# Kernel optimization log

Hardware: AMD Instinct MI355X
Metric: run time of the kernel (lower is better)

Reference implementation:

```python
import jax, jax.numpy as jnp
import numpy as np

B, D, NUM_IDS = 4096, 256, 100000
MARGIN = 0.5


def setup_inputs() -> dict:
    key = jax.random.key(0)
    k1, k2, k3, k4 = jax.random.split(key, 4)
    ftr = jax.random.normal(k1, (B, D), dtype=jnp.float32)
    teachor_ftr = jax.random.normal(k2, (B, D), dtype=jnp.float32)
    prototypes = jax.random.normal(k3, (NUM_IDS, D), dtype=jnp.float32)
    label = jax.random.randint(k4, (B,), 0, NUM_IDS, dtype=jnp.int64)
    return {"ftr": ftr, "teachor_ftr": teachor_ftr, "prototypes": prototypes, "label": label}


def reference(ftr, teachor_ftr, prototypes, label):
    # y = prototypes[label] : [B, D]
    y = prototypes[label]
    # similarity = ftr @ ftr.T : [B, B]
    sim = jnp.einsum('bd,kd->bk', ftr, ftr)
    n = ftr.shape[0]
    idx = jnp.arange(n)
    # Original: ascending sort, take first batch index i with i != label[row].
    # Equivalent: argmin of sim with positions where batch-index == label masked out.
    masked = jnp.where(idx[None, :] == label[:, None], jnp.inf, sim)
    neg_i = jnp.argmin(masked, axis=1)          # [B]
    neg = ftr[neg_i]                            # [B, D]
    pos_d = jnp.sum((ftr - y) ** 2, axis=1)     # [B]
    neg_d = jnp.sum((ftr - neg) ** 2, axis=1)   # [B]
    losses = jax.nn.relu(pos_d - neg_d + MARGIN)
    # sum(losses) / len(losses)
    return jnp.mean(losses)
```

## Files before the change

kernel.cpp:

```cpp
#include <hip/hip_runtime.h>
#include <hip/hip_bf16.h>
#include <stdint.h>


typedef _Float16 f16;
typedef _Float16 f16x4 __attribute__((ext_vector_type(4)));
typedef _Float16 f16x8 __attribute__((ext_vector_type(8)));
typedef float f32x4 __attribute__((ext_vector_type(4)));
typedef unsigned long long u64;

__device__ __forceinline__ u64 float_key(float x) {
    unsigned int u = __float_as_uint(x);
    u = (u & 0x80000000u) ? ~u : (u | 0x80000000u);
    return (u64)u;
}

__device__ __forceinline__ u64 shfl_xor_u64(u64 v, int mask) {
    unsigned int lo = (unsigned int)(v & 0xFFFFFFFFULL);
    unsigned int hi = (unsigned int)(v >> 32);
    lo = __shfl_xor(lo, mask, 64);
    hi = __shfl_xor(hi, mask, 64);
    return ((u64)hi << 32) | (u64)lo;
}

__device__ __forceinline__ void async_load16(const void* g, void* lds) {
    __builtin_amdgcn_global_load_lds(
        (__attribute__((address_space(1))) void*)(g),
        (__attribute__((address_space(3))) void*)(lds),
        16, 0, 0);
}

__global__ __launch_bounds__(256) void prep_kernel(
    const float* __restrict__ x, f16* __restrict__ F,
    u64* __restrict__ best, float* __restrict__ out, int B, int D)
{
    int gid = blockIdx.x * blockDim.x + threadIdx.x;
    int n4 = (B * D) >> 2;
    if (gid < n4) {
        float4 v = ((const float4*)x)[gid];
        f16x4 h = { (f16)v.x, (f16)v.y, (f16)v.z, (f16)v.w };
        ((f16x4*)F)[gid] = h;
    }
    if (gid < B) best[gid] = ~0ULL;
    if (gid == 0) out[0] = 0.0f;
}

__global__ __launch_bounds__(256, 3) void sim_mfma_kernel(
    const f16* __restrict__ F, const int* __restrict__ label,
    u64* __restrict__ best, int B, int K)
{
    __shared__ __align__(16) f16 sA[128 * 64];
    __shared__ __align__(16) f16 sB[128 * 64];
    __shared__ int sLabR[128];
    __shared__ int sLabC[128];

    int bi = blockIdx.x;
    int by = (int)((sqrtf(8.0f * (float)bi + 1.0f) - 1.0f) * 0.5f);
    while ((by + 1) * (by + 2) / 2 <= bi) ++by;
    while (by * (by + 1) / 2 > bi) --by;
    const int bx = bi - by * (by + 1) / 2;

    const int row0 = by * 128;
    const int col0 = bx * 128;

    const int tid  = threadIdx.x;
    const int lane = tid & 63;
    const int w    = tid >> 6;

    if (tid < 128) sLabR[tid] = label[row0 + tid];
    else           sLabC[tid - 128] = label[col0 + (tid - 128)];

    const int srow   = w * 32 + (lane >> 3);
    const int schunk = ((lane & 7) ^ (lane >> 3)) << 3;
    const f16* gA = F + (size_t)(row0 + srow) * K + schunk;
    const f16* gB = F + (size_t)(col0 + srow) * K + schunk;
    f16* lA0 = sA + (w * 32) * 64;
    f16* lB0 = sB + (w * 32) * 64;

    f32x4 acc[4][4];
#pragma unroll
    for (int i = 0; i < 4; ++i)
#pragma unroll
        for (int j = 0; j < 4; ++j) acc[i][j] = (f32x4){0.f, 0.f, 0.f, 0.f};

    const int wr = (w >> 1) * 64;
    const int wc = (w & 1) * 64;
    const int qk = lane >> 4;
    const int ln = lane & 15;

    for (int k0 = 0; k0 < K; k0 += 64) {
        __syncthreads();
#pragma unroll
        for (int t = 0; t < 4; ++t) {
            async_load16(gA + (size_t)(t * 8) * K + k0, lA0 + t * 8 * 64);
            async_load16(gB + (size_t)(t * 8) * K + k0, lB0 + t * 8 * 64);
        }
        __syncthreads();

#pragma unroll
        for (int kk = 0; kk < 2; ++kk) {
            const int q  = kk * 4 + qk;
            const int cs = ((q ^ (ln & 7)) << 3);
            f16x8 aF[4], bF[4];
#pragma unroll
            for (int f = 0; f < 4; ++f) {
                const int lrA = wr + f * 16 + ln;
                const int lrB = wc + f * 16 + ln;
                aF[f] = __builtin_bit_cast(f16x8, *(const uint4*)&sA[lrA * 64 + cs]);
                bF[f] = __builtin_bit_cast(f16x8, *(const uint4*)&sB[lrB * 64 + cs]);
            }
#pragma unroll
            for (int i = 0; i < 4; ++i)
#pragma unroll
                for (int j = 0; j < 4; ++j)
                    acc[i][j] = __builtin_amdgcn_mfma_f32_16x16x32_f16(
                        aF[i], bF[j], acc[i][j], 0, 0, 0);
        }
    }

#pragma unroll
    for (int i = 0; i < 4; ++i) {
#pragma unroll
        for (int reg = 0; reg < 4; ++reg) {
            const int lr  = wr + i * 16 + qk * 4 + reg;
            const int lab = sLabR[lr];
            u64 bl = ~0ULL;
#pragma unroll
            for (int j = 0; j < 4; ++j) {
                const int c = col0 + wc + j * 16 + ln;
                u64 key = (float_key(acc[i][j][reg]) << 32) | (unsigned int)c;
                if (c != lab && key < bl) bl = key;
            }
#pragma unroll
            for (int off = 1; off < 16; off <<= 1) {
                u64 o = shfl_xor_u64(bl, off);
                if (o < bl) bl = o;
            }
            if (ln == 0) atomicMin(&best[row0 + lr], bl);
        }
    }

#pragma unroll
    for (int j = 0; j < 4; ++j) {
        const int cl  = wc + j * 16 + ln;
        const int lab = sLabC[cl];
        u64 bl = ~0ULL;
#pragma unroll
        for (int i = 0; i < 4; ++i) {
#pragma unroll
            for (int reg = 0; reg < 4; ++reg) {
                const int rg = row0 + wr + i * 16 + qk * 4 + reg;
                u64 key = (float_key(acc[i][j][reg]) << 32) | (unsigned int)rg;
                if (rg != lab && key < bl) bl = key;
            }
        }
#pragma unroll
        for (int off = 16; off < 64; off <<= 1) {
            u64 o = shfl_xor_u64(bl, off);
            if (o < bl) bl = o;
        }
        if (qk == 0) atomicMin(&best[col0 + cl], bl);
    }
}

__global__ __launch_bounds__(256) void loss_kernel(
    const float* __restrict__ ftr, const float* __restrict__ proto,
    const int* __restrict__ label, const u64* __restrict__ best,
    float* __restrict__ out, int B, int D, float inv_b)
{
    const int gid  = blockIdx.x * blockDim.x + threadIdx.x;
    const int row  = gid >> 6;
    const int lane = gid & 63;
    if (row >= B) return;

    const int lab = label[row];
    const int neg = (int)(unsigned int)(best[row] & 0xFFFFFFFFULL);

    float pd = 0.0f, nd = 0.0f;
    for (int d = lane * 4; d < D; d += 256) {
        float4 f = *(const float4*)(ftr   + (size_t)row * D + d);
        float4 y = *(const float4*)(proto + (size_t)lab * D + d);
        float4 n = *(const float4*)(ftr   + (size_t)neg * D + d);
        float dx = f.x - y.x, dy = f.y - y.y, dz = f.z - y.z, dw = f.w - y.w;
        pd += dx * dx + dy * dy + dz * dz + dw * dw;
        dx = f.x - n.x; dy = f.y - n.y; dz = f.z - n.z; dw = f.w - n.w;
        nd += dx * dx + dy * dy + dz * dz + dw * dw;
    }
#pragma unroll
    for (int off = 32; off >= 1; off >>= 1) {
        pd += __shfl_xor(pd, off, 64);
        nd += __shfl_xor(nd, off, 64);
    }
    if (lane == 0) {
        float l = pd - nd + 0.5f;
        if (l > 0.0f) atomicAdd(out, l * inv_b);
    }
}

extern "C" void kernel_launch(void* const* d_in, const int* in_sizes, int n_in,
                              void* d_out, int out_size, void* d_ws, size_t ws_size,
                              hipStream_t stream) {
    const float* ftr   = (const float*)d_in[0];
    const float* proto = (const float*)d_in[2];
    const int*   label = (const int*)d_in[3];

    const int B = in_sizes[3];
    const int D = in_sizes[0] / B;

    u64* best = (u64*)d_ws;
    size_t off = ((size_t)B * 8 + 255) & ~(size_t)255;
    f16* F = (f16*)((char*)d_ws + off);
    float* out = (float*)d_out;

    const int prep_threads = (B * D) >> 2;
    prep_kernel<<<(prep_threads + 255) / 256, 256, 0, stream>>>(ftr, F, best, out, B, D);

    const int nb = B / 128;
    const int ntri = nb * (nb + 1) / 2;
    sim_mfma_kernel<<<ntri, 256, 0, stream>>>(F, label, best, B, D);

    loss_kernel<<<(B * 64 + 255) / 256, 256, 0, stream>>>(ftr, proto, label, best, out, B, D,
                                                          1.0f / (float)B);
}
```

Baseline: 152.9 us.

## Fuse prep, similarity and loss into one cooperative kernel with grid syncs

Merges the three kernels into a single cooperative launch that separates the prep, similarity and loss phases with grid-wide syncs, falling back to separate launches when the triangular grid cannot be co-resident. It also stages per-row and per-column argmin candidates in shared memory so each block issues one atomicMin per row or column instead of one per wave. Diagonal tiles now skip the redundant column pass. Launch overhead and atomic traffic go down, but grid syncs, per-call occupancy queries and grid-stride loops over a smaller grid in the prep and loss phases are added.

```diff
diff --git a/kernel.cpp b/kernel.cpp
--- a/kernel.cpp
+++ b/kernel.cpp
@@ -1,6 +1,9 @@
 #include <hip/hip_runtime.h>
 #include <hip/hip_bf16.h>
+#include <hip/hip_cooperative_groups.h>
 #include <stdint.h>
+
+namespace cg = cooperative_groups;
 
 
 typedef _Float16 f16;
@@ -30,22 +33,24 @@
         16, 0, 0);
 }
 
-__global__ __launch_bounds__(256) void prep_kernel(
+__device__ __forceinline__ void phase_prep(
     const float* __restrict__ x, f16* __restrict__ F,
     u64* __restrict__ best, float* __restrict__ out, int B, int D)
 {
-    int gid = blockIdx.x * blockDim.x + threadIdx.x;
-    int n4 = (B * D) >> 2;
-    if (gid < n4) {
-        float4 v = ((const float4*)x)[gid];
+    const int nthreads = gridDim.x * blockDim.x;
+    const int gid = blockIdx.x * blockDim.x + threadIdx.x;
+    const int n4 = (B * D) >> 2;
+    for (int i = gid; i < n4; i += nthreads) {
+        float4 v = ((const float4*)x)[i];
         f16x4 h = { (f16)v.x, (f16)v.y, (f16)v.z, (f16)v.w };
-        ((f16x4*)F)[gid] = h;
-    }
-    if (gid < B) best[gid] = ~0ULL;
-    if (gid == 0) out[0] = 0.0f;
-}
-
-__global__ __launch_bounds__(256, 3) void sim_mfma_kernel(
+        ((f16x4*)F)[i] = h;
+    }
+    for (int i = gid; i < B; i += nthreads) best[i] = ~0ULL;
+    if (gid == 0)
+        __hip_atomic_store(out, 0.0f, __ATOMIC_RELAXED, __HIP_MEMORY_SCOPE_AGENT);
+}
+
+__device__ __forceinline__ void phase_sim(
     const f16* __restrict__ F, const int* __restrict__ label,
     u64* __restrict__ best, int B, int K)
 {
@@ -53,12 +58,15 @@
     __shared__ __align__(16) f16 sB[128 * 64];
     __shared__ int sLabR[128];
     __shared__ int sLabC[128];
+    __shared__ u64 sRedR[2][128];
+    __shared__ u64 sRedC[2][128];
 
     int bi = blockIdx.x;
     int by = (int)((sqrtf(8.0f * (float)bi + 1.0f) - 1.0f) * 0.5f);
     while ((by + 1) * (by + 2) / 2 <= bi) ++by;
     while (by * (by + 1) / 2 > bi) --by;
     const int bx = bi - by * (by + 1) / 2;
+    const bool diag = (bx == by);
 
     const int row0 = by * 128;
     const int col0 = bx * 128;
@@ -104,10 +112,8 @@
             f16x8 aF[4], bF[4];
 #pragma unroll
             for (int f = 0; f < 4; ++f) {
-                const int lrA = wr + f * 16 + ln;
-                const int lrB = wc + f * 16 + ln;
-                aF[f] = __builtin_bit_cast(f16x8, *(const uint4*)&sA[lrA * 64 + cs]);
-                bF[f] = __builtin_bit_cast(f16x8, *(const uint4*)&sB[lrB * 64 + cs]);
+                aF[f] = __builtin_bit_cast(f16x8, *(const uint4*)&sA[(wr + f * 16 + ln) * 64 + cs]);
+                bF[f] = __builtin_bit_cast(f16x8, *(const uint4*)&sB[(wc + f * 16 + ln) * 64 + cs]);
             }
 #pragma unroll
             for (int i = 0; i < 4; ++i)
@@ -136,65 +142,113 @@
                 u64 o = shfl_xor_u64(bl, off);
                 if (o < bl) bl = o;
             }
-            if (ln == 0) atomicMin(&best[row0 + lr], bl);
-        }
-    }
-
-#pragma unroll
-    for (int j = 0; j < 4; ++j) {
-        const int cl  = wc + j * 16 + ln;
-        const int lab = sLabC[cl];
-        u64 bl = ~0ULL;
-#pragma unroll
-        for (int i = 0; i < 4; ++i) {
-#pragma unroll
-            for (int reg = 0; reg < 4; ++reg) {
-                const int rg = row0 + wr + i * 16 + qk * 4 + reg;
-                u64 key = (float_key(acc[i][j][reg]) << 32) | (unsigned int)rg;
-                if (rg != lab && key < bl) bl = key;
-            }
-        }
-#pragma unroll
-        for (int off = 16; off < 64; off <<= 1) {
-            u64 o = shfl_xor_u64(bl, off);
-            if (o < bl) bl = o;
-        }
-        if (qk == 0) atomicMin(&best[col0 + cl], bl);
-    }
+            if (ln == 0) sRedR[w & 1][lr] = bl;
+        }
+    }
+
+    if (!diag) {
+#pragma unroll
+        for (int j = 0; j < 4; ++j) {
+            const int cl  = wc + j * 16 + ln;
+            const int lab = sLabC[cl];
+            u64 bl = ~0ULL;
+#pragma unroll
+            for (int i = 0; i < 4; ++i) {
+#pragma unroll
+                for (int reg = 0; reg < 4; ++reg) {
+                    const int rg = row0 + wr + i * 16 + qk * 4 + reg;
+                    u64 key = (float_key(acc[i][j][reg]) << 32) | (unsigned int)rg;
+                    if (rg != lab && key < bl) bl = key;
+                }
+            }
+            u64 o = shfl_xor_u64(bl, 16); if (o < bl) bl = o;
+            o     = shfl_xor_u64(bl, 32); if (o < bl) bl = o;
+            if (qk == 0) sRedC[w >> 1][cl] = bl;
+        }
+    }
+
+    __syncthreads();
+    if (tid < 128) {
+        u64 a = sRedR[0][tid], b = sRedR[1][tid];
+        atomicMin(&best[row0 + tid], a < b ? a : b);
+    } else if (!diag) {
+        const int c = tid - 128;
+        u64 a = sRedC[0][c], b = sRedC[1][c];
+        atomicMin(&best[col0 + c], a < b ? a : b);
+    }
+}
+
+__device__ __forceinline__ void phase_loss(
+    const float* __restrict__ ftr, const float* __restrict__ proto,
+    const int* __restrict__ label, u64* __restrict__ best,
+    float* __restrict__ out, int B, int D, float inv_b)
+{
+    const int nwaves = gridDim.x * (blockDim.x >> 6);
+    const int wid0   = blockIdx.x * (blockDim.x >> 6) + (threadIdx.x >> 6);
+    const int lane   = threadIdx.x & 63;
+
+    for (int row = wid0; row < B; row += nwaves) {
+        const int lab = label[row];
+        const u64 bk  = __hip_atomic_load(&best[row], __ATOMIC_RELAXED,
+                                          __HIP_MEMORY_SCOPE_AGENT);
+        const int neg = (int)(unsigned int)(bk & 0xFFFFFFFFULL);
+
+        float pd = 0.0f, nd = 0.0f;
+        for (int d = lane * 4; d < D; d += 256) {
+            float4 f = *(const float4*)(ftr   + (size_t)row * D + d);
+            float4 y = *(const float4*)(proto + (size_t)lab * D + d);
+            float4 n = *(const float4*)(ftr   + (size_t)neg * D + d);
+            float dx = f.x - y.x, dy = f.y - y.y, dz = f.z - y.z, dw = f.w - y.w;
+            pd += dx * dx + dy * dy + dz * dz + dw * dw;
+            dx = f.x - n.x; dy = f.y - n.y; dz = f.z - n.z; dw = f.w - n.w;
+            nd += dx * dx + dy * dy + dz * dz + dw * dw;
+        }
+#pragma unroll
+        for (int off = 32; off >= 1; off >>= 1) {
+            pd += __shfl_xor(pd, off, 64);
+            nd += __shfl_xor(nd, off, 64);
+        }
+        if (lane == 0) {
+            float l = pd - nd + 0.5f;
+            if (l > 0.0f) atomicAdd(out, l * inv_b);
+        }
+    }
+}
+
+__global__ __launch_bounds__(256, 3) void fused_kernel(
+    const float* __restrict__ ftr, const float* __restrict__ proto,
+    const int* __restrict__ label, f16* __restrict__ F,
+    u64* __restrict__ best, float* __restrict__ out,
+    int B, int D, float inv_b)
+{
+    cg::grid_group g = cg::this_grid();
+    phase_prep(ftr, F, best, out, B, D);
+    g.sync();
+    phase_sim(F, label, best, B, D);
+    g.sync();
+    phase_loss(ftr, proto, label, best, out, B, D, inv_b);
+}
+
+__global__ __launch_bounds__(256) void prep_kernel(
+    const float* __restrict__ x, f16* __restrict__ F,
+    u64* __restrict__ best, float* __restrict__ out, int B, int D)
+{
+    phase_prep(x, F, best, out, B, D);
+}
+
+__global__ __launch_bounds__(256, 3) void sim_kernel(
+    const f16* __restrict__ F, const int* __restrict__ label,
+    u64* __restrict__ best, int B, int K)
+{
+    phase_sim(F, label, best, B, K);
 }
 
 __global__ __launch_bounds__(256) void loss_kernel(
     const float* __restrict__ ftr, const float* __restrict__ proto,
-    const int* __restrict__ label, const u64* __restrict__ best,
+    const int* __restrict__ label, u64* __restrict__ best,
     float* __restrict__ out, int B, int D, float inv_b)
 {
-    const int gid  = blockIdx.x * blockDim.x + threadIdx.x;
-    const int row  = gid >> 6;
-    const int lane = gid & 63;
-    if (row >= B) return;
-
-    const int lab = label[row];
-    const int neg = (int)(unsigned int)(best[row] & 0xFFFFFFFFULL);
-
-    float pd = 0.0f, nd = 0.0f;
-    for (int d = lane * 4; d < D; d += 256) {
-        float4 f = *(const float4*)(ftr   + (size_t)row * D + d);
-        float4 y = *(const float4*)(proto + (size_t)lab * D + d);
-        float4 n = *(const float4*)(ftr   + (size_t)neg * D + d);
-        float dx = f.x - y.x, dy = f.y - y.y, dz = f.z - y.z, dw = f.w - y.w;
-        pd += dx * dx + dy * dy + dz * dz + dw * dw;
-        dx = f.x - n.x; dy = f.y - n.y; dz = f.z - n.z; dw = f.w - n.w;
-        nd += dx * dx + dy * dy + dz * dz + dw * dw;
-    }
-#pragma unroll
-    for (int off = 32; off >= 1; off >>= 1) {
-        pd += __shfl_xor(pd, off, 64);
-        nd += __shfl_xor(nd, off, 64);
-    }
-    if (lane == 0) {
-        float l = pd - nd + 0.5f;
-        if (l > 0.0f) atomicAdd(out, l * inv_b);
-    }
+    phase_loss(ftr, proto, label, best, out, B, D, inv_b);
 }
 
 extern "C" void kernel_launch(void* const* d_in, const int* in_sizes, int n_in,
@@ -211,14 +265,28 @@
     size_t off = ((size_t)B * 8 + 255) & ~(size_t)255;
     f16* F = (f16*)((char*)d_ws + off);
     float* out = (float*)d_out;
-
-    const int prep_threads = (B * D) >> 2;
-    prep_kernel<<<(prep_threads + 255) / 256, 256, 0, stream>>>(ftr, F, best, out, B, D);
-
-    const int nb = B / 128;
+    float inv_b = 1.0f / (float)B;
+
+    const int nb   = B / 128;
     const int ntri = nb * (nb + 1) / 2;
-    sim_mfma_kernel<<<ntri, 256, 0, stream>>>(F, label, best, B, D);
-
-    loss_kernel<<<(B * 64 + 255) / 256, 256, 0, stream>>>(ftr, proto, label, best, out, B, D,
-                                                          1.0f / (float)B);
-}
+
+    int blocksPerCU = 0, numCU = 0, dev = 0;
+    (void)hipGetDevice(&dev);
+    (void)hipDeviceGetAttribute(&numCU, hipDeviceAttributeMultiprocessorCount, dev);
+    (void)hipOccupancyMaxActiveBlocksPerMultiprocessor(&blocksPerCU, fused_kernel, 256, 0);
+    const bool coop = (blocksPerCU > 0 && numCU > 0 &&
+                       (long long)blocksPerCU * numCU >= (long long)ntri);
+
+    if (coop) {
+        void* args[] = { (void*)&ftr, (void*)&proto, (void*)&label, (void*)&F,
+                         (void*)&best, (void*)&out, (void*)&B, (void*)&D, (void*)&inv_b };
+        (void)hipLaunchCooperativeKernel((void*)fused_kernel, dim3(ntri), dim3(256),
+                                         args, 0, stream);
+    } else {
+        const int prep_threads = (B * D) >> 2;
+        prep_kernel<<<(prep_threads + 255) / 256, 256, 0, stream>>>(ftr, F, best, out, B, D);
+        sim_kernel<<<ntri, 256, 0, stream>>>(F, label, best, B, D);
+        loss_kernel<<<(B * 64 + 255) / 256, 256, 0, stream>>>(ftr, proto, label, best, out,
+                                                              B, D, inv_b);
+    }
+}
```

Result: no change. 153.8 us (+0.6%).

## Fuse fp16 conversion into sim kernel and replace atomics with per-tile partial minima

Applied to the files above, without the earlier changes.

Removes the separate prep kernel by converting fp32 features to fp16 on the fly while staging tiles into LDS, using swizzled vector stores in place of async global-to-LDS loads. Replaces per-row global 64-bit atomicMin with an in-block LDS reduction that writes one partial minimum per (row, tile) into a B×32 workspace. The loss kernel then reduces the 32 partials per row itself, so the best array no longer needs initialising. Output zeroing moves into the sim kernel. In exchange, each tile re-reads fp32 data (twice the bytes) and converts it redundantly, and the loads are now synchronous register loads instead of async copies.

```diff
diff --git a/kernel.cpp b/kernel.cpp
--- a/kernel.cpp
+++ b/kernel.cpp
@@ -4,7 +4,6 @@
 
 
 typedef _Float16 f16;
-typedef _Float16 f16x4 __attribute__((ext_vector_type(4)));
 typedef _Float16 f16x8 __attribute__((ext_vector_type(8)));
 typedef float f32x4 __attribute__((ext_vector_type(4)));
 typedef unsigned long long u64;
@@ -23,42 +22,23 @@
     return ((u64)hi << 32) | (u64)lo;
 }
 
-__device__ __forceinline__ void async_load16(const void* g, void* lds) {
-    __builtin_amdgcn_global_load_lds(
-        (__attribute__((address_space(1))) void*)(g),
-        (__attribute__((address_space(3))) void*)(lds),
-        16, 0, 0);
-}
-
-__global__ __launch_bounds__(256) void prep_kernel(
-    const float* __restrict__ x, f16* __restrict__ F,
-    u64* __restrict__ best, float* __restrict__ out, int B, int D)
-{
-    int gid = blockIdx.x * blockDim.x + threadIdx.x;
-    int n4 = (B * D) >> 2;
-    if (gid < n4) {
-        float4 v = ((const float4*)x)[gid];
-        f16x4 h = { (f16)v.x, (f16)v.y, (f16)v.z, (f16)v.w };
-        ((f16x4*)F)[gid] = h;
-    }
-    if (gid < B) best[gid] = ~0ULL;
-    if (gid == 0) out[0] = 0.0f;
-}
-
-__global__ __launch_bounds__(256, 3) void sim_mfma_kernel(
-    const f16* __restrict__ F, const int* __restrict__ label,
-    u64* __restrict__ best, int B, int K)
+__global__ __launch_bounds__(256, 3) void sim_kernel(
+    const float* __restrict__ ftr, const int* __restrict__ label,
+    u64* __restrict__ P, float* __restrict__ out, int B, int D)
 {
     __shared__ __align__(16) f16 sA[128 * 64];
     __shared__ __align__(16) f16 sB[128 * 64];
     __shared__ int sLabR[128];
     __shared__ int sLabC[128];
+    __shared__ u64 sRedR[2][128];
+    __shared__ u64 sRedC[2][128];
 
     int bi = blockIdx.x;
     int by = (int)((sqrtf(8.0f * (float)bi + 1.0f) - 1.0f) * 0.5f);
     while ((by + 1) * (by + 2) / 2 <= bi) ++by;
     while (by * (by + 1) / 2 > bi) --by;
     const int bx = bi - by * (by + 1) / 2;
+    const bool diag = (bx == by);
 
     const int row0 = by * 128;
     const int col0 = bx * 128;
@@ -67,15 +47,13 @@
     const int lane = tid & 63;
     const int w    = tid >> 6;
 
+    if (tid == 0)
+        __hip_atomic_store(out, 0.0f, __ATOMIC_RELAXED, __HIP_MEMORY_SCOPE_AGENT);
     if (tid < 128) sLabR[tid] = label[row0 + tid];
     else           sLabC[tid - 128] = label[col0 + (tid - 128)];
 
-    const int srow   = w * 32 + (lane >> 3);
-    const int schunk = ((lane & 7) ^ (lane >> 3)) << 3;
-    const f16* gA = F + (size_t)(row0 + srow) * K + schunk;
-    const f16* gB = F + (size_t)(col0 + srow) * K + schunk;
-    f16* lA0 = sA + (w * 32) * 64;
-    f16* lB0 = sB + (w * 32) * 64;
+    const int srow = tid >> 3;
+    const int skc  = tid & 7;
 
     f32x4 acc[4][4];
 #pragma unroll
@@ -88,12 +66,28 @@
     const int qk = lane >> 4;
     const int ln = lane & 15;
 
-    for (int k0 = 0; k0 < K; k0 += 64) {
+    for (int k0 = 0; k0 < D; k0 += 64) {
         __syncthreads();
 #pragma unroll
         for (int t = 0; t < 4; ++t) {
-            async_load16(gA + (size_t)(t * 8) * K + k0, lA0 + t * 8 * 64);
-            async_load16(gB + (size_t)(t * 8) * K + k0, lB0 + t * 8 * 64);
+            const int r = srow + t * 32;
+            const int ldsoff = r * 64 + (((skc ^ (r & 7)) << 3));
+            {
+                const float* g = ftr + (size_t)(row0 + r) * D + k0 + skc * 8;
+                float4 a0 = *(const float4*)g;
+                float4 a1 = *(const float4*)(g + 4);
+                f16x8 h = { (f16)a0.x, (f16)a0.y, (f16)a0.z, (f16)a0.w,
+                            (f16)a1.x, (f16)a1.y, (f16)a1.z, (f16)a1.w };
+                *(f16x8*)&sA[ldsoff] = h;
+            }
+            {
+                const float* g = ftr + (size_t)(col0 + r) * D + k0 + skc * 8;
+                float4 b0 = *(const float4*)g;
+                float4 b1 = *(const float4*)(g + 4);
+                f16x8 h = { (f16)b0.x, (f16)b0.y, (f16)b0.z, (f16)b0.w,
+                            (f16)b1.x, (f16)b1.y, (f16)b1.z, (f16)b1.w };
+                *(f16x8*)&sB[ldsoff] = h;
+            }
         }
         __syncthreads();
 
@@ -104,10 +98,8 @@
             f16x8 aF[4], bF[4];
 #pragma unroll
             for (int f = 0; f < 4; ++f) {
-                const int lrA = wr + f * 16 + ln;
-                const int lrB = wc + f * 16 + ln;
-                aF[f] = __builtin_bit_cast(f16x8, *(const uint4*)&sA[lrA * 64 + cs]);
-                bF[f] = __builtin_bit_cast(f16x8, *(const uint4*)&sB[lrB * 64 + cs]);
+                aF[f] = __builtin_bit_cast(f16x8, *(const uint4*)&sA[(wr + f * 16 + ln) * 64 + cs]);
+                bF[f] = __builtin_bit_cast(f16x8, *(const uint4*)&sB[(wc + f * 16 + ln) * 64 + cs]);
             }
 #pragma unroll
             for (int i = 0; i < 4; ++i)
@@ -136,36 +128,45 @@
                 u64 o = shfl_xor_u64(bl, off);
                 if (o < bl) bl = o;
             }
-            if (ln == 0) atomicMin(&best[row0 + lr], bl);
-        }
-    }
-
-#pragma unroll
-    for (int j = 0; j < 4; ++j) {
-        const int cl  = wc + j * 16 + ln;
-        const int lab = sLabC[cl];
-        u64 bl = ~0ULL;
-#pragma unroll
-        for (int i = 0; i < 4; ++i) {
-#pragma unroll
-            for (int reg = 0; reg < 4; ++reg) {
-                const int rg = row0 + wr + i * 16 + qk * 4 + reg;
-                u64 key = (float_key(acc[i][j][reg]) << 32) | (unsigned int)rg;
-                if (rg != lab && key < bl) bl = key;
-            }
-        }
-#pragma unroll
-        for (int off = 16; off < 64; off <<= 1) {
-            u64 o = shfl_xor_u64(bl, off);
-            if (o < bl) bl = o;
-        }
-        if (qk == 0) atomicMin(&best[col0 + cl], bl);
+            if (ln == 0) sRedR[w & 1][lr] = bl;
+        }
+    }
+
+    if (!diag) {
+#pragma unroll
+        for (int j = 0; j < 4; ++j) {
+            const int cl  = wc + j * 16 + ln;
+            const int lab = sLabC[cl];
+            u64 bl = ~0ULL;
+#pragma unroll
+            for (int i = 0; i < 4; ++i) {
+#pragma unroll
+                for (int reg = 0; reg < 4; ++reg) {
+                    const int rg = row0 + wr + i * 16 + qk * 4 + reg;
+                    u64 key = (float_key(acc[i][j][reg]) << 32) | (unsigned int)rg;
+                    if (rg != lab && key < bl) bl = key;
+                }
+            }
+            u64 o = shfl_xor_u64(bl, 16); if (o < bl) bl = o;
+            o     = shfl_xor_u64(bl, 32); if (o < bl) bl = o;
+            if (qk == 0) sRedC[w >> 1][cl] = bl;
+        }
+    }
+
+    __syncthreads();
+    if (tid < 128) {
+        u64 a = sRedR[0][tid], b = sRedR[1][tid];
+        P[(size_t)(row0 + tid) * 32 + bx] = (a < b ? a : b);
+    } else if (!diag) {
+        const int c = tid - 128;
+        u64 a = sRedC[0][c], b = sRedC[1][c];
+        P[(size_t)(col0 + c) * 32 + by] = (a < b ? a : b);
     }
 }
 
 __global__ __launch_bounds__(256) void loss_kernel(
     const float* __restrict__ ftr, const float* __restrict__ proto,
-    const int* __restrict__ label, const u64* __restrict__ best,
+    const int* __restrict__ label, const u64* __restrict__ P,
     float* __restrict__ out, int B, int D, float inv_b)
 {
     const int gid  = blockIdx.x * blockDim.x + threadIdx.x;
@@ -173,8 +174,14 @@
     const int lane = gid & 63;
     if (row >= B) return;
 
+    u64 bl = (lane < 32) ? P[(size_t)row * 32 + lane] : ~0ULL;
+#pragma unroll
+    for (int off = 32; off >= 1; off >>= 1) {
+        u64 o = shfl_xor_u64(bl, off);
+        if (o < bl) bl = o;
+    }
+    const int neg = (int)(unsigned int)(bl & 0xFFFFFFFFULL);
     const int lab = label[row];
-    const int neg = (int)(unsigned int)(best[row] & 0xFFFFFFFFULL);
 
     float pd = 0.0f, nd = 0.0f;
     for (int d = lane * 4; d < D; d += 256) {
@@ -207,18 +214,13 @@
     const int B = in_sizes[3];
     const int D = in_sizes[0] / B;
 
-    u64* best = (u64*)d_ws;
-    size_t off = ((size_t)B * 8 + 255) & ~(size_t)255;
-    f16* F = (f16*)((char*)d_ws + off);
+    u64* P = (u64*)d_ws;
     float* out = (float*)d_out;
 
-    const int prep_threads = (B * D) >> 2;
-    prep_kernel<<<(prep_threads + 255) / 256, 256, 0, stream>>>(ftr, F, best, out, B, D);
-
-    const int nb = B / 128;
+    const int nb   = B / 128;
     const int ntri = nb * (nb + 1) / 2;
-    sim_mfma_kernel<<<ntri, 256, 0, stream>>>(F, label, best, B, D);
-
-    loss_kernel<<<(B * 64 + 255) / 256, 256, 0, stream>>>(ftr, proto, label, best, out, B, D,
+
+    sim_kernel<<<ntri, 256, 0, stream>>>(ftr, label, P, out, B, D);
+    loss_kernel<<<(B * 64 + 255) / 256, 256, 0, stream>>>(ftr, proto, label, P, out, B, D,
                                                           1.0f / (float)B);
 }
```

Measured after the change: 176.1 us. 15.1% more time.

## Replace global atomicMin with per-tile partial argmin buffer reduced in loss kernel

Applied to the files above, without the earlier changes.

Each sim tile now reduces its row and column argmin candidates in shared memory and writes one value per row and column into a partial buffer P[B][32] with plain stores, replacing the 64-bit global atomicMin calls. The loss kernel reduces the 32 partials per row with wavefront shuffles, and best no longer needs initialising in the prep kernel. Diagonal tiles skip the redundant column pass. This removes contention on global 64-bit atomics and adds a shared-memory sync plus a larger workspace. P is sized with a hardcoded stride of 32, which ties it to B/128 == 32.

```diff
diff --git a/kernel.cpp b/kernel.cpp
--- a/kernel.cpp
+++ b/kernel.cpp
@@ -31,8 +31,8 @@
 }
 
 __global__ __launch_bounds__(256) void prep_kernel(
-    const float* __restrict__ x, f16* __restrict__ F,
-    u64* __restrict__ best, float* __restrict__ out, int B, int D)
+    const float* __restrict__ x, f16* __restrict__ F, float* __restrict__ out,
+    int B, int D)
 {
     int gid = blockIdx.x * blockDim.x + threadIdx.x;
     int n4 = (B * D) >> 2;
@@ -41,24 +41,26 @@
         f16x4 h = { (f16)v.x, (f16)v.y, (f16)v.z, (f16)v.w };
         ((f16x4*)F)[gid] = h;
     }
-    if (gid < B) best[gid] = ~0ULL;
     if (gid == 0) out[0] = 0.0f;
 }
 
-__global__ __launch_bounds__(256, 3) void sim_mfma_kernel(
+__global__ __launch_bounds__(256, 3) void sim_kernel(
     const f16* __restrict__ F, const int* __restrict__ label,
-    u64* __restrict__ best, int B, int K)
+    u64* __restrict__ P, int B, int K)
 {
     __shared__ __align__(16) f16 sA[128 * 64];
     __shared__ __align__(16) f16 sB[128 * 64];
     __shared__ int sLabR[128];
     __shared__ int sLabC[128];
+    __shared__ u64 sRedR[2][128];
+    __shared__ u64 sRedC[2][128];
 
     int bi = blockIdx.x;
     int by = (int)((sqrtf(8.0f * (float)bi + 1.0f) - 1.0f) * 0.5f);
     while ((by + 1) * (by + 2) / 2 <= bi) ++by;
     while (by * (by + 1) / 2 > bi) --by;
     const int bx = bi - by * (by + 1) / 2;
+    const bool diag = (bx == by);
 
     const int row0 = by * 128;
     const int col0 = bx * 128;
@@ -104,10 +106,8 @@
             f16x8 aF[4], bF[4];
 #pragma unroll
             for (int f = 0; f < 4; ++f) {
-                const int lrA = wr + f * 16 + ln;
-                const int lrB = wc + f * 16 + ln;
-                aF[f] = __builtin_bit_cast(f16x8, *(const uint4*)&sA[lrA * 64 + cs]);
-                bF[f] = __builtin_bit_cast(f16x8, *(const uint4*)&sB[lrB * 64 + cs]);
+                aF[f] = __builtin_bit_cast(f16x8, *(const uint4*)&sA[(wr + f * 16 + ln) * 64 + cs]);
+                bF[f] = __builtin_bit_cast(f16x8, *(const uint4*)&sB[(wc + f * 16 + ln) * 64 + cs]);
             }
 #pragma unroll
             for (int i = 0; i < 4; ++i)
@@ -136,36 +136,45 @@
                 u64 o = shfl_xor_u64(bl, off);
                 if (o < bl) bl = o;
             }
-            if (ln == 0) atomicMin(&best[row0 + lr], bl);
-        }
-    }
-
-#pragma unroll
-    for (int j = 0; j < 4; ++j) {
-        const int cl  = wc + j * 16 + ln;
-        const int lab = sLabC[cl];
-        u64 bl = ~0ULL;
-#pragma unroll
-        for (int i = 0; i < 4; ++i) {
-#pragma unroll
-            for (int reg = 0; reg < 4; ++reg) {
-                const int rg = row0 + wr + i * 16 + qk * 4 + reg;
-                u64 key = (float_key(acc[i][j][reg]) << 32) | (unsigned int)rg;
-                if (rg != lab && key < bl) bl = key;
-            }
-        }
-#pragma unroll
-        for (int off = 16; off < 64; off <<= 1) {
-            u64 o = shfl_xor_u64(bl, off);
-            if (o < bl) bl = o;
-        }
-        if (qk == 0) atomicMin(&best[col0 + cl], bl);
+            if (ln == 0) sRedR[w & 1][lr] = bl;
+        }
+    }
+
+    if (!diag) {
+#pragma unroll
+        for (int j = 0; j < 4; ++j) {
+            const int cl  = wc + j * 16 + ln;
+            const int lab = sLabC[cl];
+            u64 bl = ~0ULL;
+#pragma unroll
+            for (int i = 0; i < 4; ++i) {
+#pragma unroll
+                for (int reg = 0; reg < 4; ++reg) {
+                    const int rg = row0 + wr + i * 16 + qk * 4 + reg;
+                    u64 key = (float_key(acc[i][j][reg]) << 32) | (unsigned int)rg;
+                    if (rg != lab && key < bl) bl = key;
+                }
+            }
+            u64 o = shfl_xor_u64(bl, 16); if (o < bl) bl = o;
+            o     = shfl_xor_u64(bl, 32); if (o < bl) bl = o;
+            if (qk == 0) sRedC[w >> 1][cl] = bl;
+        }
+    }
+
+    __syncthreads();
+    if (tid < 128) {
+        u64 a = sRedR[0][tid], b = sRedR[1][tid];
+        P[(size_t)(row0 + tid) * 32 + bx] = (a < b ? a : b);
+    } else if (!diag) {
+        const int c = tid - 128;
+        u64 a = sRedC[0][c], b = sRedC[1][c];
+        P[(size_t)(col0 + c) * 32 + by] = (a < b ? a : b);
     }
 }
 
 __global__ __launch_bounds__(256) void loss_kernel(
     const float* __restrict__ ftr, const float* __restrict__ proto,
-    const int* __restrict__ label, const u64* __restrict__ best,
+    const int* __restrict__ label, const u64* __restrict__ P,
     float* __restrict__ out, int B, int D, float inv_b)
 {
     const int gid  = blockIdx.x * blockDim.x + threadIdx.x;
@@ -173,8 +182,18 @@
     const int lane = gid & 63;
     if (row >= B) return;
 
+    u64 bl = (lane < 32) ? P[(size_t)row * 32 + lane] : ~0ULL;
+#pragma unroll
+    for (int off = 16; off >= 1; off >>= 1) {
+        u64 o = shfl_xor_u64(bl, off);
+        if (o < bl) bl = o;
+    }
+    {
+        u64 o = shfl_xor_u64(bl, 32);
+        if (o < bl) bl = o;
+    }
+    const int neg = (int)(unsigned int)(bl & 0xFFFFFFFFULL);
     const int lab = label[row];
-    const int neg = (int)(unsigned int)(best[row] & 0xFFFFFFFFULL);
 
     float pd = 0.0f, nd = 0.0f;
     for (int d = lane * 4; d < D; d += 256) {
@@ -207,18 +226,18 @@
     const int B = in_sizes[3];
     const int D = in_sizes[0] / B;
 
-    u64* best = (u64*)d_ws;
-    size_t off = ((size_t)B * 8 + 255) & ~(size_t)255;
+    u64* P = (u64*)d_ws;
+    size_t off = ((size_t)B * 32 * 8 + 255) & ~(size_t)255;
     f16* F = (f16*)((char*)d_ws + off);
     float* out = (float*)d_out;
 
     const int prep_threads = (B * D) >> 2;
-    prep_kernel<<<(prep_threads + 255) / 256, 256, 0, stream>>>(ftr, F, best, out, B, D);
-
-    const int nb = B / 128;
+    prep_kernel<<<(prep_threads + 255) / 256, 256, 0, stream>>>(ftr, F, out, B, D);
+
+    const int nb   = B / 128;
     const int ntri = nb * (nb + 1) / 2;
-    sim_mfma_kernel<<<ntri, 256, 0, stream>>>(F, label, best, B, D);
-
-    loss_kernel<<<(B * 64 + 255) / 256, 256, 0, stream>>>(ftr, proto, label, best, out, B, D,
+    sim_kernel<<<ntri, 256, 0, stream>>>(F, label, P, B, D);
+
+    loss_kernel<<<(B * 64 + 255) / 256, 256, 0, stream>>>(ftr, proto, label, P, out, B, D,
                                                           1.0f / (float)B);
 }
```

Measured after the change: 155.6 us. No clear change (+1.7%).
